# Kernel optimization log

Hardware: AMD Instinct MI355X
Metric: run time of the kernel (lower is better)

Reference implementation:

```python
import jax, jax.numpy as jnp
import numpy as np

NUM_HEADS = 8
ATTN_DIM = 64

def setup_inputs() -> dict:
    key = jax.random.key(0)
    ks = jax.random.split(key, 16)
    C = ATTN_DIM
    inp = {
        "rgb_fea": jax.random.normal(ks[0], (2, C, 48, 48), jnp.float32),
        "depth_fea": jax.random.normal(ks[1], (2, 1, 24, 24), jnp.float32),
        # expend_conv: Conv2d(1 -> C, k=1), with bias (torch default)
        "w_exp": jax.random.normal(ks[2], (C, 1), jnp.float32) * 0.2,
        "b_exp": jax.random.normal(ks[3], (C,), jnp.float32) * 0.02,
        # q/k/v linears (no bias), weights stored torch-style [out, in]
        "w_rgb_q": jax.random.normal(ks[4], (C, C), jnp.float32) * (C ** -0.5),
        "w_rgb_k": jax.random.normal(ks[5], (C, C), jnp.float32) * (C ** -0.5),
        "w_rgb_v": jax.random.normal(ks[6], (C, C), jnp.float32) * (C ** -0.5),
        "w_dep_q": jax.random.normal(ks[7], (C, C), jnp.float32) * (C ** -0.5),
        "w_dep_k": jax.random.normal(ks[8], (C, C), jnp.float32) * (C ** -0.5),
        "w_dep_v": jax.random.normal(ks[9], (C, C), jnp.float32) * (C ** -0.5),
        # output projections (with bias)
        "w_rgb_proj": jax.random.normal(ks[10], (C, C), jnp.float32) * (C ** -0.5),
        "b_rgb_proj": jax.random.normal(ks[11], (C,), jnp.float32) * 0.02,
        "w_dep_proj": jax.random.normal(ks[12], (C, C), jnp.float32) * (C ** -0.5),
        "b_dep_proj": jax.random.normal(ks[13], (C,), jnp.float32) * 0.02,
        # compress_conv: Conv2d(2C -> C, k=1), with bias
        "w_comp": jax.random.normal(ks[14], (C, 2 * C), jnp.float32) * ((2 * C) ** -0.5),
        "b_comp": jax.random.normal(ks[15], (C,), jnp.float32) * 0.02,
    }
    return inp


def _heads(x, b, n, h):
    # [B, N, C] -> [B, H, N, C/H]
    c = x.shape[-1]
    return x.reshape(b, n, h, c // h).transpose(0, 2, 1, 3)


def reference(rgb_fea, depth_fea, w_exp, b_exp,
              w_rgb_q, w_rgb_k, w_rgb_v, w_dep_q, w_dep_k, w_dep_v,
              w_rgb_proj, b_rgb_proj, w_dep_proj, b_dep_proj,
              w_comp, b_comp):
    b, c, h, w = rgb_fea.shape
    H = NUM_HEADS
    scale = (c // H) ** -0.5

    # expend_conv (1x1) + ReLU + bilinear upsample (align_corners=False)
    d = jnp.einsum('bihw,oi->bohw', depth_fea, w_exp) + b_exp[None, :, None, None]
    d = jax.nn.relu(d)
    d = jax.image.resize(d, (b, c, h, w), method='bilinear')

    # (B,C,H,W) -> transpose(1,3) -> (B,W,H,C) -> (B, N=w*h, C)
    N = w * h
    rgb = rgb_fea.transpose(0, 3, 2, 1).reshape(b, N, c)
    dep = d.transpose(0, 3, 2, 1).reshape(b, N, c)

    rq = _heads(rgb @ w_rgb_q.T, b, N, H)
    rk = _heads(rgb @ w_rgb_k.T, b, N, H)
    rv = _heads(rgb @ w_rgb_v.T, b, N, H)
    dq = _heads(dep @ w_dep_q.T, b, N, H)
    dk = _heads(dep @ w_dep_k.T, b, N, H)
    dv = _heads(dep @ w_dep_v.T, b, N, H)

    # rgb queries attend to depth keys/values
    rgb_attn = jax.nn.softmax(jnp.einsum('bhnd,bhmd->bhnm', rq, dk) * scale, axis=-1)
    rgb_out = jnp.einsum('bhnm,bhmd->bhnd', rgb_attn, dv)
    rgb_out = rgb_out.transpose(0, 2, 1, 3).reshape(b, N, c) @ w_rgb_proj.T + b_rgb_proj

    # depth queries attend to rgb keys/values
    dep_attn = jax.nn.softmax(jnp.einsum('bhnd,bhmd->bhnm', dq, rk) * scale, axis=-1)
    dep_out = jnp.einsum('bhnm,bhmd->bhnd', dep_attn, rv)
    dep_out = dep_out.transpose(0, 2, 1, 3).reshape(b, N, c) @ w_dep_proj.T + b_dep_proj

    # (B,N,C) -> (B,C,N) -> (B,C,w,h)
    rgb_out = rgb_out.transpose(0, 2, 1).reshape(b, c, w, h)
    dep_out = dep_out.transpose(0, 2, 1).reshape(b, c, w, h)

    fuse = jnp.concatenate([rgb_out, dep_out], axis=1)
    fuse = jnp.einsum('bihw,oi->bohw', fuse, w_comp) + b_comp[None, :, None, None]
    return jax.nn.gelu(fuse, approximate=False)
```

## Files before the change

kernel.cpp:

```cpp
#include <hip/hip_runtime.h>
#include <math.h>

#define BATCH 2
#define C 64
#define HH 48
#define WW 48
#define NTOK 2304
#define HEADS 8
#define KVSTRIDE 12

typedef unsigned short bf16_t;
typedef __attribute__((ext_vector_type(8))) short bf16x8;
typedef __attribute__((ext_vector_type(4))) short bf16x4;
typedef __attribute__((ext_vector_type(4))) float f32x4;

__device__ __forceinline__ bf16_t f2bf(float f) {
    unsigned int u = __float_as_uint(f);
    u = (u + 0x7fffu + ((u >> 16) & 1u)) >> 16;
    return (bf16_t)u;
}
__device__ __forceinline__ unsigned pack2(float a, float b) {
    return (unsigned)f2bf(a) | ((unsigned)f2bf(b) << 16);
}
__device__ __forceinline__ float4 ld_bf4(const bf16_t* p) {
    uint2 v = *(const uint2*)p;
    float4 r;
    r.x = __uint_as_float(v.x << 16); r.y = __uint_as_float(v.x & 0xffff0000u);
    r.z = __uint_as_float(v.y << 16); r.w = __uint_as_float(v.y & 0xffff0000u);
    return r;
}

__device__ __forceinline__ void stage_x_row(
    float* xrow, const float* rgb, const float* dep,
    const float* w_exp, const float* b_exp,
    int b, int n, int strm, int c0, int cstep)
{
    int wi = n / HH, hi = n % HH;
    if (strm == 0) {
        const float* base = rgb + (size_t)b * C * NTOK + (size_t)hi * WW + wi;
        for (int c = c0; c < 64; c += cstep)
            xrow[c] = base[(size_t)c * NTOK];
    } else {
        float cy = 0.5f * hi - 0.25f, cx = 0.5f * wi - 0.25f;
        float fy0 = floorf(cy), fx0 = floorf(cx);
        float fy = cy - fy0, fx = cx - fx0;
        int y0 = max((int)fy0, 0), x0 = max((int)fx0, 0);
        int y1 = min((int)fy0 + 1, 23), x1 = min((int)fx0 + 1, 23);
        const float* dp = dep + b * 576;
        float d00 = dp[y0*24 + x0], d01 = dp[y0*24 + x1];
        float d10 = dp[y1*24 + x0], d11 = dp[y1*24 + x1];
        for (int c = c0; c < 64; c += cstep) {
            float w = w_exp[c], bb = b_exp[c];
            float r00 = fmaxf(w*d00 + bb, 0.f), r01 = fmaxf(w*d01 + bb, 0.f);
            float r10 = fmaxf(w*d10 + bb, 0.f), r11 = fmaxf(w*d11 + bb, 0.f);
            xrow[c] = (1.f-fy)*((1.f-fx)*r00 + fx*r01) + fy*((1.f-fx)*r10 + fx*r11);
        }
    }
}


__global__ __launch_bounds__(256) void qkvprep_kernel(
    const float* __restrict__ rgb, const float* __restrict__ dep,
    const float* __restrict__ w_exp, const float* __restrict__ b_exp,
    const float* __restrict__ w_rq, const float* __restrict__ w_rk,
    const float* __restrict__ w_rv,
    const float* __restrict__ w_dq, const float* __restrict__ w_dk,
    const float* __restrict__ w_dv,
    const float* __restrict__ w_rp, const float* __restrict__ w_dp,
    const float* __restrict__ w_comp,
    const float* __restrict__ b_rp, const float* __restrict__ b_dp,
    const float* __restrict__ b_comp,
    bf16_t* __restrict__ Qb, bf16_t* __restrict__ Kb, bf16_t* __restrict__ VT,
    float* __restrict__ W1, float* __restrict__ W2, float* __restrict__ beff)
{
    __shared__ float Xs[16][68];
    __shared__ float Ws[64][68];
    int bxid = blockIdx.x;
    int tid = threadIdx.x;
    int sr = tid >> 4, sc = (tid & 15) * 4;

    if (bxid < 144) {
        int tile = bxid;
        int z = blockIdx.y;
        int b = z >> 1, strm = z & 1;
        int sb = strm*2 + b;

        float4 wreg[3][4];
        #pragma unroll
        for (int m = 0; m < 3; ++m) {
            const float* W = strm ? (m == 0 ? w_dq : m == 1 ? w_dk : w_dv)
                                  : (m == 0 ? w_rq : m == 1 ? w_rk : w_rv);
            #pragma unroll
            for (int rr = 0; rr < 4; ++rr)
                wreg[m][rr] = *(const float4*)&W[(rr*16 + sr)*64 + sc];
        }
        {
            int r = tid & 15, c0 = tid >> 4;
            stage_x_row(&Xs[r][0], rgb, dep, w_exp, b_exp,
                        b, tile*16 + r, strm, c0, 16);
        }

        int ty = tid >> 4, tx = tid & 15;
        #pragma unroll
        for (int m = 0; m < 3; ++m) {
            __syncthreads();
            #pragma unroll
            for (int rr = 0; rr < 4; ++rr)
                *(float4*)&Ws[rr*16 + sr][sc] = wreg[m][rr];
            __syncthreads();

            float acc[4] = {};
            #pragma unroll
            for (int k = 0; k < 64; k += 4) {
                float4 xv = *(const float4*)&Xs[ty][k];
                #pragma unroll
                for (int j = 0; j < 4; ++j) {
                    float4 wv = *(const float4*)&Ws[tx + 16*j][k];
                    acc[j] += xv.x*wv.x + xv.y*wv.y + xv.z*wv.z + xv.w*wv.w;
                }
            }
            float scale = (m == 0) ? (0.35355339059327373f * 1.4426950408889634f) : 1.0f;
            int n = tile*16 + ty;
            #pragma unroll
            for (int j = 0; j < 4; ++j) {
                int o = tx + 16*j;
                int h = o >> 3, d = o & 7;
                bf16_t v = f2bf(acc[j] * scale);
                if (m == 0)      Qb[(((size_t)sb*8 + h)*NTOK + n)*8 + d] = v;
                else if (m == 1) Kb[(((size_t)sb*8 + h)*NTOK + n)*8 + d] = v;
                else             VT[(((size_t)sb*8 + h)*8 + d)*NTOK + n] = v;
            }
        }
    } else {
        int m = bxid - 144;
        int bx = blockIdx.y;
        const float* Wp = m ? w_dp : w_rp;
        float* Wo = m ? W2 : W1;
        #pragma unroll
        for (int rr = 0; rr < 4; ++rr) {
            int r = rr*16 + sr;
            *(float4*)&Ws[r][sc] = *(const float4*)&Wp[r*64 + sc];
        }
        __syncthreads();
        int r = tid >> 4;
        int o = bx*16 + r;
        int c4 = (tid & 15) * 4;
        float a0 = 0, a1 = 0, a2 = 0, a3 = 0;
        for (int j = 0; j < 64; ++j) {
            float wc = w_comp[o*128 + m*64 + j];
            float4 wp = *(const float4*)&Ws[j][c4];
            a0 += wc*wp.x; a1 += wc*wp.y; a2 += wc*wp.z; a3 += wc*wp.w;
        }
        Wo[o*64 + c4]     = a0;
        Wo[o*64 + c4 + 1] = a1;
        Wo[o*64 + c4 + 2] = a2;
        Wo[o*64 + c4 + 3] = a3;
        if (m == 0 && bx == 0 && tid < 64) {
            float s = b_comp[tid];
            for (int j = 0; j < 64; ++j)
                s += w_comp[tid*128 + j] * b_rp[j] + w_comp[tid*128 + 64 + j] * b_dp[j];
            beff[tid] = s;
        }
    }
}

__global__ __launch_bounds__(256) void attn_kernel(
    const bf16_t* __restrict__ Qb, const bf16_t* __restrict__ Kb,
    const bf16_t* __restrict__ VT,
    float* __restrict__ AOr, float* __restrict__ AOd)
{
    int h = blockIdx.y;
    int z = blockIdx.z;
    int b = z >> 1, which = z & 1;
    int qsb = which * 2 + b;
    int ksb = (1 - which) * 2 + b;
    const bf16_t* Q  = Qb + ((size_t)qsb * 8 + h) * NTOK * 8;
    const bf16_t* K  = Kb + ((size_t)ksb * 8 + h) * NTOK * 8;
    const bf16_t* Vt = VT + ((size_t)ksb * 8 + h) * 8 * NTOK;
    float* AO = which ? AOd : AOr;

    __shared__ __align__(16) bf16_t Pls[4][16][40];
    __shared__ __align__(16) float  Ols[4][16][16];

    int tid = threadIdx.x;
    int t = tid & 63, w = tid >> 6;
    int m16 = t & 15, quad = t >> 4;
    int qt = blockIdx.x * 4 + w;
    int n0 = qt * 16;

    const bf16x8 zf = {0,0,0,0,0,0,0,0};
    const bf16x8 onesf = {0x3F80,0x3F80,0x3F80,0x3F80,
                          0x3F80,0x3F80,0x3F80,0x3F80};
    const f32x4 cz = {0.f, 0.f, 0.f, 0.f};

    bf16x8 qf = (quad == 0) ? *(const bf16x8*)&Q[(size_t)(n0 + m16) * 8] : zf;

    f32x4 oacc = cz;

    #pragma unroll 1
    for (int ck = 0; ck < 72; ++ck) {
        int k0 = ck * 32;
        bf16x8 kf0 = (quad == 0) ? *(const bf16x8*)&K[(size_t)(k0 + m16) * 8]      : zf;
        bf16x8 kf1 = (quad == 0) ? *(const bf16x8*)&K[(size_t)(k0 + 16 + m16) * 8] : zf;
        bf16x8 vf = (m16 < 8) ? *(const bf16x8*)&Vt[(size_t)m16 * NTOK + k0 + quad * 8]
                  : (m16 == 8 ? onesf : zf);

        f32x4 s0 = __builtin_amdgcn_mfma_f32_16x16x32_bf16(kf0, qf, cz, 0, 0, 0);
        f32x4 s1 = __builtin_amdgcn_mfma_f32_16x16x32_bf16(kf1, qf, cz, 0, 0, 0);

        bf16x4 pA, pB;
        #pragma unroll
        for (int r = 0; r < 4; ++r) {
            float p0 = __builtin_amdgcn_exp2f(s0[r]);
            float p1 = __builtin_amdgcn_exp2f(s1[r]);
            pA[r] = (short)(__float_as_uint(p0) >> 16);
            pB[r] = (short)(__float_as_uint(p1) >> 16);
        }
        *(bf16x4*)&Pls[w][m16][quad * 4]      = pA;
        *(bf16x4*)&Pls[w][m16][16 + quad * 4] = pB;

        bf16x8 pf = *(const bf16x8*)&Pls[w][m16][quad * 8];
        oacc = __builtin_amdgcn_mfma_f32_16x16x32_bf16(pf, vf, oacc, 0, 0, 0);
    }

    #pragma unroll
    for (int r = 0; r < 4; ++r)
        Ols[w][quad*4 + r][m16] = oacc[r];
    #pragma unroll
    for (int e = 0; e < 2; ++e) {
        int idx = t * 2 + e;
        int qq = idx >> 3, d = idx & 7;
        float val = Ols[w][qq][d] / Ols[w][qq][8];
        AO[((size_t)b * NTOK + n0 + qq) * 64 + 8 * h + d] = val;
    }
}

__global__ __launch_bounds__(256) void outcomp_kernel(
    const float* __restrict__ AOr, const float* __restrict__ AOd,
    const float* __restrict__ W1, const float* __restrict__ W2,
    const float* __restrict__ beff, float* __restrict__ out)
{
    int tile = blockIdx.x;
    int b    = blockIdx.y;
    int n0 = tile * 16;
    __shared__ float Ar[16][68];
    __shared__ float Ad[16][68];
    __shared__ float W1s[64][68];
    __shared__ float W2s[64][68];
    int tid = threadIdx.x;
    {
        int row = tid >> 4, c4 = (tid & 15) * 4;
        size_t base = (size_t)b*NTOK + n0 + row;
        *(float4*)&Ar[row][c4] = *(const float4*)&AOr[base*64 + c4];
        *(float4*)&Ad[row][c4] = *(const float4*)&AOd[base*64 + c4];
    }
    {
        int sr = tid >> 4, sc4 = (tid & 15) * 4;
        #pragma unroll
        for (int rr = 0; rr < 4; ++rr) {
            int r = rr*16 + sr;
            *(float4*)&W1s[r][sc4] = *(const float4*)&W1[r*64 + sc4];
            *(float4*)&W2s[r][sc4] = *(const float4*)&W2[r*64 + sc4];
        }
    }
    __syncthreads();

    int tx = tid & 15, ty = tid >> 4;
    float g[4] = {};
    #pragma unroll
    for (int k = 0; k < 64; k += 4) {
        float4 xr = *(const float4*)&Ar[ty][k];
        float4 xd = *(const float4*)&Ad[ty][k];
        #pragma unroll
        for (int jj = 0; jj < 4; ++jj) {
            float4 w1 = *(const float4*)&W1s[tx + 16*jj][k];
            float4 w2 = *(const float4*)&W2s[tx + 16*jj][k];
            g[jj] += xr.x*w1.x + xr.y*w1.y + xr.z*w1.z + xr.w*w1.w
                   + xd.x*w2.x + xd.y*w2.y + xd.z*w2.z + xd.w*w2.w;
        }
    }

    __syncthreads();
    float* Gs = &W1s[0][0];
    #pragma unroll
    for (int jj = 0; jj < 4; ++jj) {
        int o = tx + 16*jj;
        float x = g[jj] + beff[o];
        float gl = 0.5f * x * (1.0f + erff(x * 0.70710678118654752f));
        Gs[o*20 + ty] = gl;
    }
    __syncthreads();
    {
        int o = tid >> 2, s = tid & 3;
        float4 v = *(const float4*)&Gs[o*20 + 4*s];
        *(float4*)&out[((size_t)(b*C + o))*NTOK + n0 + 4*s] = v;
    }
}

__global__ __launch_bounds__(256) void kv_all_kernel(
    const float* __restrict__ rgb, const float* __restrict__ dep,
    const float* __restrict__ w_exp, const float* __restrict__ b_exp,
    const float* __restrict__ w_rk, const float* __restrict__ w_rv,
    const float* __restrict__ w_dk, const float* __restrict__ w_dv,
    bf16_t* __restrict__ Kr, bf16_t* __restrict__ Vr,
    bf16_t* __restrict__ Kd, bf16_t* __restrict__ Vd)
{
    int tile = blockIdx.x;
    int m    = blockIdx.y;
    int z    = blockIdx.z;
    int b = z >> 1, strm = z & 1;
    const float* W = strm ? (m ? w_dv : w_dk) : (m ? w_rv : w_rk);
    bf16_t* O = (strm ? (m ? Vd : Kd) : (m ? Vr : Kr))
              + ((size_t)b * NTOK + tile * 64) * 64;

    __shared__ float Xs[64][68];
    __shared__ float Ws[64][68];
    int tid = threadIdx.x;
    {
        int r = tid & 63, c0 = tid >> 6;
        stage_x_row(&Xs[r][0], rgb, dep, w_exp, b_exp, b, tile*64 + r, strm, c0, 4);
    }
    int sr = tid >> 4, sc = (tid & 15) * 4;
    #pragma unroll
    for (int rr = 0; rr < 4; ++rr) {
        int r = rr*16 + sr;
        *(float4*)&Ws[r][sc] = *(const float4*)&W[r*64 + sc];
    }
    __syncthreads();

    int ty = tid >> 4, tx = tid & 15;
    float acc[4][4] = {};
    #pragma unroll
    for (int k = 0; k < 64; k += 4) {
        float4 xv[4], wv4[4];
        #pragma unroll
        for (int i = 0; i < 4; ++i) xv[i] = *(const float4*)&Xs[4*ty + i][k];
        #pragma unroll
        for (int j = 0; j < 4; ++j) wv4[j] = *(const float4*)&Ws[tx + 16*j][k];
        #pragma unroll
        for (int i = 0; i < 4; ++i)
            #pragma unroll
            for (int j = 0; j < 4; ++j)
                acc[i][j] += xv[i].x*wv4[j].x + xv[i].y*wv4[j].y + xv[i].z*wv4[j].z + xv[i].w*wv4[j].w;
    }
    #pragma unroll
    for (int i = 0; i < 4; ++i)
        #pragma unroll
        for (int j = 0; j < 4; ++j)
            O[(4*ty + i)*64 + tx + 16*j] = f2bf(acc[i][j]);
}

__global__ __launch_bounds__(256) void attn_all_kernel(
    const float* __restrict__ rgb, const float* __restrict__ dep,
    const float* __restrict__ w_exp, const float* __restrict__ b_exp,
    const float* __restrict__ w_rq, const float* __restrict__ w_dq,
    const bf16_t* __restrict__ Kr, const bf16_t* __restrict__ Vr,
    const bf16_t* __restrict__ Kd, const bf16_t* __restrict__ Vd,
    bf16_t* __restrict__ AOr, bf16_t* __restrict__ AOd)
{
    int qt = blockIdx.x;
    int h  = blockIdx.y;
    int z  = blockIdx.z;
    int b = z >> 1, which = z & 1;
    const float* wq = which ? w_dq : w_rq;
    const bf16_t* K = which ? Kr : Kd;
    const bf16_t* V = which ? Vr : Vd;
    bf16_t* AO      = which ? AOd : AOr;

    __shared__ float Xs[64][68];
    __shared__ float Wqs[8][64];
    __shared__ __align__(16) float Ks[4][64][KVSTRIDE];
    __shared__ __align__(16) float Vs[4][64][KVSTRIDE];

    int tid = threadIdx.x;
    int t = tid & 63;
    int w = tid >> 6;
    int n = qt * 64 + t;

    stage_x_row(&Xs[t][0], rgb, dep, w_exp, b_exp, b, n, which == 0 ? 0 : 1, w, 4);
    if (w == 0) {
        #pragma unroll
        for (int d = 0; d < 8; ++d) Wqs[d][t] = wq[(8*h + d)*64 + t];
    }
    __syncthreads();

    const float sc = 0.35355339059327373f * 1.4426950408889634f;
    float q[8];
    #pragma unroll
    for (int d = 0; d < 8; ++d) {
        float s = 0.f;
        #pragma unroll 8
        for (int c = 0; c < 64; ++c) s += Xs[t][c] * Wqs[d][c];
        q[d] = s * sc;
    }

    float mrun = -INFINITY, l = 0.f;
    float acc[8] = {};

    #pragma unroll 1
    for (int st = 0; st < 9; ++st) {
        __syncthreads();
        {
            size_t g = ((size_t)b * NTOK + (w*576 + st*64 + t)) * 64 + 8 * h;
            *(float4*)&Ks[w][t][0] = ld_bf4(&K[g]);
            *(float4*)&Ks[w][t][4] = ld_bf4(&K[g + 4]);
            *(float4*)&Vs[w][t][0] = ld_bf4(&V[g]);
            *(float4*)&Vs[w][t][4] = ld_bf4(&V[g + 4]);
        }
        __syncthreads();

        for (int g8 = 0; g8 < 8; ++g8) {
            float s[8];
            #pragma unroll
            for (int u = 0; u < 8; ++u) {
                const float4 ka = *(const float4*)&Ks[w][g8*8 + u][0];
                const float4 kb = *(const float4*)&Ks[w][g8*8 + u][4];
                s[u] = q[0]*ka.x + q[1]*ka.y + q[2]*ka.z + q[3]*ka.w
                     + q[4]*kb.x + q[5]*kb.y + q[6]*kb.z + q[7]*kb.w;
            }
            float tm = fmaxf(fmaxf(fmaxf(s[0],s[1]), fmaxf(s[2],s[3])),
                             fmaxf(fmaxf(s[4],s[5]), fmaxf(s[6],s[7])));
            float mn = fmaxf(mrun, tm);
            float alpha = __builtin_amdgcn_exp2f(mrun - mn);
            float ps = 0.f;
            #pragma unroll
            for (int u = 0; u < 8; ++u) { s[u] = __builtin_amdgcn_exp2f(s[u] - mn); ps += s[u]; }
            l = l * alpha + ps;
            #pragma unroll
            for (int d = 0; d < 8; ++d) acc[d] *= alpha;
            #pragma unroll
            for (int u = 0; u < 8; ++u) {
                const float4 va = *(const float4*)&Vs[w][g8*8 + u][0];
                const float4 vb = *(const float4*)&Vs[w][g8*8 + u][4];
                acc[0] += s[u]*va.x; acc[1] += s[u]*va.y; acc[2] += s[u]*va.z; acc[3] += s[u]*va.w;
                acc[4] += s[u]*vb.x; acc[5] += s[u]*vb.y; acc[6] += s[u]*vb.z; acc[7] += s[u]*vb.w;
            }
            mrun = mn;
        }
    }

    float* part = &Xs[0][0];
    __syncthreads();
    {
        float* p = &part[(w*64 + t) * 10];
        p[0] = mrun; p[1] = l;
        #pragma unroll
        for (int d = 0; d < 8; ++d) p[2 + d] = acc[d];
    }
    __syncthreads();
    if (tid < 64) {
        float M = -INFINITY;
        #pragma unroll
        for (int v = 0; v < 4; ++v) M = fmaxf(M, part[(v*64 + t)*10]);
        float L = 0.f, o[8] = {};
        #pragma unroll
        for (int v = 0; v < 4; ++v) {
            const float* p = &part[(v*64 + t)*10];
            float al = __builtin_amdgcn_exp2f(p[0] - M);
            L += p[1] * al;
            #pragma unroll
            for (int d = 0; d < 8; ++d) o[d] += p[2 + d] * al;
        }
        float inv = 1.0f / L;
        uint4 ov;
        ov.x = pack2(o[0]*inv, o[1]*inv);
        ov.y = pack2(o[2]*inv, o[3]*inv);
        ov.z = pack2(o[4]*inv, o[5]*inv);
        ov.w = pack2(o[6]*inv, o[7]*inv);
        *(uint4*)&AO[((size_t)b * NTOK + n) * 64 + 8 * h] = ov;
    }
}

__global__ __launch_bounds__(256) void projcomp_all_kernel(
    const bf16_t* __restrict__ AOr, const bf16_t* __restrict__ AOd,
    const float* __restrict__ w_rp, const float* __restrict__ b_rp,
    const float* __restrict__ w_dp, const float* __restrict__ b_dp,
    const float* __restrict__ w_comp, const float* __restrict__ b_comp,
    float* __restrict__ out)
{
    int tile = blockIdx.x;
    int b    = blockIdx.y;
    __shared__ float A[64][68];
    __shared__ float Bf[64][68];
    __shared__ float Pf[64][68];
    int tid = threadIdx.x;
    int sr = tid >> 4, sc = (tid & 15) * 4;
    int ty = tid >> 4, tx = tid & 15;
    float G[4][4] = {};

    #pragma unroll
    for (int half = 0; half < 2; ++half) {
        const bf16_t* AOx = half ? AOd : AOr;
        const float* Wp   = half ? w_dp : w_rp;
        const float* bp   = half ? b_dp : b_rp;
        #pragma unroll
        for (int rr = 0; rr < 4; ++rr) {
            int r = rr*16 + sr;
            *(float4*)&A[r][sc]  = ld_bf4(&AOx[((size_t)b*NTOK + tile*64 + r)*64 + sc]);
            *(float4*)&Bf[r][sc] = *(const float4*)&Wp[r*64 + sc];
        }
        __syncthreads();
        float acc[4][4] = {};
        #pragma unroll
        for (int k = 0; k < 64; k += 4) {
            float4 xv[4], wv[4];
            #pragma unroll
            for (int i = 0; i < 4; ++i) xv[i] = *(const float4*)&A[4*ty + i][k];
            #pragma unroll
            for (int j = 0; j < 4; ++j) wv[j] = *(const float4*)&Bf[tx + 16*j][k];
            #pragma unroll
            for (int i = 0; i < 4; ++i)
                #pragma unroll
                for (int j = 0; j < 4; ++j)
                    acc[i][j] += xv[i].x*wv[j].x + xv[i].y*wv[j].y + xv[i].z*wv[j].z + xv[i].w*wv[j].w;
        }
        __syncthreads();
        #pragma unroll
        for (int j = 0; j < 4; ++j) {
            float bj = bp[tx + 16*j];
            #pragma unroll
            for (int i = 0; i < 4; ++i)
                Pf[4*ty + i][tx + 16*j] = acc[i][j] + bj;
        }
        #pragma unroll
        for (int rr = 0; rr < 4; ++rr) {
            int r = rr*16 + sr;
            *(float4*)&Bf[r][sc] = *(const float4*)&w_comp[r*128 + half*64 + sc];
        }
        __syncthreads();
        #pragma unroll
        for (int k = 0; k < 64; k += 4) {
            float4 xv[4], wv[4];
            #pragma unroll
            for (int i = 0; i < 4; ++i) xv[i] = *(const float4*)&Pf[4*ty + i][k];
            #pragma unroll
            for (int j = 0; j < 4; ++j) wv[j] = *(const float4*)&Bf[tx + 16*j][k];
            #pragma unroll
            for (int i = 0; i < 4; ++i)
                #pragma unroll
                for (int j = 0; j < 4; ++j)
                    G[i][j] += xv[i].x*wv[j].x + xv[i].y*wv[j].y + xv[i].z*wv[j].z + xv[i].w*wv[j].w;
        }
        __syncthreads();
    }

    #pragma unroll
    for (int j = 0; j < 4; ++j) {
        int o = tx + 16*j;
        float bj = b_comp[o];
        #pragma unroll
        for (int i = 0; i < 4; ++i) {
            int n = tile*64 + 4*ty + i;
            int wi = n / HH, hi = n % HH;
            float x = G[i][j] + bj;
            float g = 0.5f * x * (1.0f + erff(x * 0.70710678118654752f));
            out[((b*C + o)*WW + wi)*HH + hi] = g;
        }
    }
}

extern "C" void kernel_launch(void* const* d_in, const int* in_sizes, int n_in,
                              void* d_out, int out_size, void* d_ws, size_t ws_size,
                              hipStream_t stream) {
    const float* rgb_fea = (const float*)d_in[0];
    const float* depth   = (const float*)d_in[1];
    const float* w_exp   = (const float*)d_in[2];
    const float* b_exp   = (const float*)d_in[3];
    const float* w_rq    = (const float*)d_in[4];
    const float* w_rk    = (const float*)d_in[5];
    const float* w_rv    = (const float*)d_in[6];
    const float* w_dq    = (const float*)d_in[7];
    const float* w_dk    = (const float*)d_in[8];
    const float* w_dv    = (const float*)d_in[9];
    const float* w_rp    = (const float*)d_in[10];
    const float* b_rp    = (const float*)d_in[11];
    const float* w_dp    = (const float*)d_in[12];
    const float* b_dp    = (const float*)d_in[13];
    const float* w_comp  = (const float*)d_in[14];
    const float* b_comp  = (const float*)d_in[15];
    float* out = (float*)d_out;

    if (ws_size >= 5931264) {
        char* Wb = (char*)d_ws;
        bf16_t* Qb   = (bf16_t*)Wb;
        bf16_t* Kb   = (bf16_t*)(Wb + 1179648);
        bf16_t* VT   = (bf16_t*)(Wb + 2359296);
        float*  AOr  = (float*)(Wb + 3538944);
        float*  AOd  = AOr + 294912;
        float*  W1   = (float*)(Wb + 5898240);
        float*  W2   = (float*)(Wb + 5914624);
        float*  beff = (float*)(Wb + 5931008);

        qkvprep_kernel<<<dim3(146, 4), dim3(256), 0, stream>>>(
            rgb_fea, depth, w_exp, b_exp,
            w_rq, w_rk, w_rv, w_dq, w_dk, w_dv,
            w_rp, w_dp, w_comp, b_rp, b_dp, b_comp,
            Qb, Kb, VT, W1, W2, beff);
        attn_kernel<<<dim3(36, 8, 4), dim3(256), 0, stream>>>(
            Qb, Kb, VT, AOr, AOd);
        outcomp_kernel<<<dim3(144, 2), dim3(256), 0, stream>>>(
            AOr, AOd, W1, W2, beff, out);
    } else {
        const size_t BUF = (size_t)BATCH * NTOK * 64;
        bf16_t* Kr  = (bf16_t*)d_ws;
        bf16_t* Vr  = Kr + BUF;
        bf16_t* Kd  = Vr + BUF;
        bf16_t* Vd  = Kd + BUF;
        bf16_t* AOr = Vd + BUF;
        bf16_t* AOd = AOr + BUF;
        kv_all_kernel<<<dim3(36, 2, 4), dim3(256), 0, stream>>>(
            rgb_fea, depth, w_exp, b_exp, w_rk, w_rv, w_dk, w_dv, Kr, Vr, Kd, Vd);
        attn_all_kernel<<<dim3(36, 8, 4), dim3(256), 0, stream>>>(
            rgb_fea, depth, w_exp, b_exp, w_rq, w_dq, Kr, Vr, Kd, Vd, AOr, AOd);
        projcomp_all_kernel<<<dim3(36, 2), dim3(256), 0, stream>>>(
            AOr, AOd, w_rp, b_rp, w_dp, b_dp, w_comp, b_comp, out);
    }
}
```

Measured before the change: 161.3 us.

## Split QKV prep across grid z and unroll attention loop by two chunks

The QKV prep kernel now spreads the three projections (Q, K, V) over blockIdx.z, so each block computes a single projection with one weight-staging pass. Launch is 145x4x3, and the former two extra weight-fold blocks are remapped to block 144 with z<2. The attention kernel processes 64 keys per iteration, with double P buffers in LDS, to give more independent MFMA and exp work per loop trip. This adds more blocks that each restage the X rows, and raises register and LDS use in attention.

```diff
diff --git a/kernel.cpp b/kernel.cpp
--- a/kernel.cpp
+++ b/kernel.cpp
@@ -82,57 +82,48 @@
     if (bxid < 144) {
         int tile = bxid;
         int z = blockIdx.y;
+        int m = blockIdx.z;
         int b = z >> 1, strm = z & 1;
         int sb = strm*2 + b;
-
-        float4 wreg[3][4];
-        #pragma unroll
-        for (int m = 0; m < 3; ++m) {
-            const float* W = strm ? (m == 0 ? w_dq : m == 1 ? w_dk : w_dv)
-                                  : (m == 0 ? w_rq : m == 1 ? w_rk : w_rv);
-            #pragma unroll
-            for (int rr = 0; rr < 4; ++rr)
-                wreg[m][rr] = *(const float4*)&W[(rr*16 + sr)*64 + sc];
+        const float* W = strm ? (m == 0 ? w_dq : m == 1 ? w_dk : w_dv)
+                              : (m == 0 ? w_rq : m == 1 ? w_rk : w_rv);
+
+        #pragma unroll
+        for (int rr = 0; rr < 4; ++rr) {
+            int r = rr*16 + sr;
+            *(float4*)&Ws[r][sc] = *(const float4*)&W[r*64 + sc];
         }
         {
             int r = tid & 15, c0 = tid >> 4;
             stage_x_row(&Xs[r][0], rgb, dep, w_exp, b_exp,
                         b, tile*16 + r, strm, c0, 16);
         }
+        __syncthreads();
 
         int ty = tid >> 4, tx = tid & 15;
-        #pragma unroll
-        for (int m = 0; m < 3; ++m) {
-            __syncthreads();
-            #pragma unroll
-            for (int rr = 0; rr < 4; ++rr)
-                *(float4*)&Ws[rr*16 + sr][sc] = wreg[m][rr];
-            __syncthreads();
-
-            float acc[4] = {};
-            #pragma unroll
-            for (int k = 0; k < 64; k += 4) {
-                float4 xv = *(const float4*)&Xs[ty][k];
-                #pragma unroll
-                for (int j = 0; j < 4; ++j) {
-                    float4 wv = *(const float4*)&Ws[tx + 16*j][k];
-                    acc[j] += xv.x*wv.x + xv.y*wv.y + xv.z*wv.z + xv.w*wv.w;
-                }
+        float acc[4] = {};
+        #pragma unroll
+        for (int k = 0; k < 64; k += 4) {
+            float4 xv = *(const float4*)&Xs[ty][k];
+            #pragma unroll
+            for (int j = 0; j < 4; ++j) {
+                float4 wv = *(const float4*)&Ws[tx + 16*j][k];
+                acc[j] += xv.x*wv.x + xv.y*wv.y + xv.z*wv.z + xv.w*wv.w;
             }
-            float scale = (m == 0) ? (0.35355339059327373f * 1.4426950408889634f) : 1.0f;
-            int n = tile*16 + ty;
-            #pragma unroll
-            for (int j = 0; j < 4; ++j) {
-                int o = tx + 16*j;
-                int h = o >> 3, d = o & 7;
-                bf16_t v = f2bf(acc[j] * scale);
-                if (m == 0)      Qb[(((size_t)sb*8 + h)*NTOK + n)*8 + d] = v;
-                else if (m == 1) Kb[(((size_t)sb*8 + h)*NTOK + n)*8 + d] = v;
-                else             VT[(((size_t)sb*8 + h)*8 + d)*NTOK + n] = v;
-            }
-        }
-    } else {
-        int m = bxid - 144;
+        }
+        float scale = (m == 0) ? (0.35355339059327373f * 1.4426950408889634f) : 1.0f;
+        int n = tile*16 + ty;
+        #pragma unroll
+        for (int j = 0; j < 4; ++j) {
+            int o = tx + 16*j;
+            int h = o >> 3, d = o & 7;
+            bf16_t v = f2bf(acc[j] * scale);
+            if (m == 0)      Qb[(((size_t)sb*8 + h)*NTOK + n)*8 + d] = v;
+            else if (m == 1) Kb[(((size_t)sb*8 + h)*NTOK + n)*8 + d] = v;
+            else             VT[(((size_t)sb*8 + h)*8 + d)*NTOK + n] = v;
+        }
+    } else if (blockIdx.z < 2) {
+        int m = blockIdx.z;
         int bx = blockIdx.y;
         const float* Wp = m ? w_dp : w_rp;
         float* Wo = m ? W2 : W1;
@@ -179,7 +170,7 @@
     const bf16_t* Vt = VT + ((size_t)ksb * 8 + h) * 8 * NTOK;
     float* AO = which ? AOd : AOr;
 
-    __shared__ __align__(16) bf16_t Pls[4][16][40];
+    __shared__ __align__(16) bf16_t Pls[4][2][16][40];
     __shared__ __align__(16) float  Ols[4][16][16];
 
     int tid = threadIdx.x;
@@ -192,35 +183,51 @@
     const bf16x8 onesf = {0x3F80,0x3F80,0x3F80,0x3F80,
                           0x3F80,0x3F80,0x3F80,0x3F80};
     const f32x4 cz = {0.f, 0.f, 0.f, 0.f};
+    bf16_t* PA = &Pls[w][0][0][0];
+    bf16_t* PB = &Pls[w][1][0][0];
 
     bf16x8 qf = (quad == 0) ? *(const bf16x8*)&Q[(size_t)(n0 + m16) * 8] : zf;
 
     f32x4 oacc = cz;
 
     #pragma unroll 1
-    for (int ck = 0; ck < 72; ++ck) {
-        int k0 = ck * 32;
-        bf16x8 kf0 = (quad == 0) ? *(const bf16x8*)&K[(size_t)(k0 + m16) * 8]      : zf;
-        bf16x8 kf1 = (quad == 0) ? *(const bf16x8*)&K[(size_t)(k0 + 16 + m16) * 8] : zf;
-        bf16x8 vf = (m16 < 8) ? *(const bf16x8*)&Vt[(size_t)m16 * NTOK + k0 + quad * 8]
+    for (int ck = 0; ck < 36; ++ck) {
+        int k0 = ck * 64;
+        bf16x8 kA0 = (quad == 0) ? *(const bf16x8*)&K[(size_t)(k0 + m16) * 8]      : zf;
+        bf16x8 kA1 = (quad == 0) ? *(const bf16x8*)&K[(size_t)(k0 + 16 + m16) * 8] : zf;
+        bf16x8 kB0 = (quad == 0) ? *(const bf16x8*)&K[(size_t)(k0 + 32 + m16) * 8] : zf;
+        bf16x8 kB1 = (quad == 0) ? *(const bf16x8*)&K[(size_t)(k0 + 48 + m16) * 8] : zf;
+        bf16x8 vA = (m16 < 8) ? *(const bf16x8*)&Vt[(size_t)m16 * NTOK + k0 + quad * 8]
                   : (m16 == 8 ? onesf : zf);
-
-        f32x4 s0 = __builtin_amdgcn_mfma_f32_16x16x32_bf16(kf0, qf, cz, 0, 0, 0);
-        f32x4 s1 = __builtin_amdgcn_mfma_f32_16x16x32_bf16(kf1, qf, cz, 0, 0, 0);
-
-        bf16x4 pA, pB;
+        bf16x8 vB = (m16 < 8) ? *(const bf16x8*)&Vt[(size_t)m16 * NTOK + k0 + 32 + quad * 8]
+                  : (m16 == 8 ? onesf : zf);
+
+        f32x4 sA0 = __builtin_amdgcn_mfma_f32_16x16x32_bf16(kA0, qf, cz, 0, 0, 0);
+        f32x4 sA1 = __builtin_amdgcn_mfma_f32_16x16x32_bf16(kA1, qf, cz, 0, 0, 0);
+        f32x4 sB0 = __builtin_amdgcn_mfma_f32_16x16x32_bf16(kB0, qf, cz, 0, 0, 0);
+        f32x4 sB1 = __builtin_amdgcn_mfma_f32_16x16x32_bf16(kB1, qf, cz, 0, 0, 0);
+
+        bf16x4 pA0, pA1, pB0, pB1;
         #pragma unroll
         for (int r = 0; r < 4; ++r) {
-            float p0 = __builtin_amdgcn_exp2f(s0[r]);
-            float p1 = __builtin_amdgcn_exp2f(s1[r]);
-            pA[r] = (short)(__float_as_uint(p0) >> 16);
-            pB[r] = (short)(__float_as_uint(p1) >> 16);
-        }
-        *(bf16x4*)&Pls[w][m16][quad * 4]      = pA;
-        *(bf16x4*)&Pls[w][m16][16 + quad * 4] = pB;
-
-        bf16x8 pf = *(const bf16x8*)&Pls[w][m16][quad * 8];
-        oacc = __builtin_amdgcn_mfma_f32_16x16x32_bf16(pf, vf, oacc, 0, 0, 0);
+            float a0 = __builtin_amdgcn_exp2f(sA0[r]);
+            float a1 = __builtin_amdgcn_exp2f(sA1[r]);
+            float b0 = __builtin_amdgcn_exp2f(sB0[r]);
+            float b1 = __builtin_amdgcn_exp2f(sB1[r]);
+            pA0[r] = (short)(__float_as_uint(a0) >> 16);
+            pA1[r] = (short)(__float_as_uint(a1) >> 16);
+            pB0[r] = (short)(__float_as_uint(b0) >> 16);
+            pB1[r] = (short)(__float_as_uint(b1) >> 16);
+        }
+        *(bf16x4*)&PA[m16*40 + quad * 4]      = pA0;
+        *(bf16x4*)&PA[m16*40 + 16 + quad * 4] = pA1;
+        *(bf16x4*)&PB[m16*40 + quad * 4]      = pB0;
+        *(bf16x4*)&PB[m16*40 + 16 + quad * 4] = pB1;
+
+        bf16x8 pfA = *(const bf16x8*)&PA[m16*40 + quad * 8];
+        oacc = __builtin_amdgcn_mfma_f32_16x16x32_bf16(pfA, vA, oacc, 0, 0, 0);
+        bf16x8 pfB = *(const bf16x8*)&PB[m16*40 + quad * 8];
+        oacc = __builtin_amdgcn_mfma_f32_16x16x32_bf16(pfB, vB, oacc, 0, 0, 0);
     }
 
     #pragma unroll
@@ -591,7 +598,7 @@
         float*  W2   = (float*)(Wb + 5914624);
         float*  beff = (float*)(Wb + 5931008);
 
-        qkvprep_kernel<<<dim3(146, 4), dim3(256), 0, stream>>>(
+        qkvprep_kernel<<<dim3(145, 4, 3), dim3(256), 0, stream>>>(
             rgb_fea, depth, w_exp, b_exp,
             w_rq, w_rk, w_rv, w_dq, w_dk, w_dv,
             w_rp, w_dp, w_comp, b_rp, b_dp, b_comp,
```

Result: slower. 167.0 us (+3.5%).

## Fuse output projection and GELU into attention via last-arriver counters

Applied to the files above, without the earlier changes.

Removes the separate outcomp kernel. Each attention wave increments a per-(batch, query-tile) atomic counter, and the 16th arriver (8 heads × 2 directions) performs the folded projection, compress conv and GELU for that 16-token tile. Counters are zeroed in the prep kernel, which now also splits the Q/K/V projections across a third grid dimension so each block computes one matrix. This saves a kernel launch and its tail, at the cost of atomics, fences, and a scalar per-wave epilogue that reads weights from global memory.

```diff
diff --git a/kernel.cpp b/kernel.cpp
--- a/kernel.cpp
+++ b/kernel.cpp
@@ -71,7 +71,8 @@
     const float* __restrict__ b_rp, const float* __restrict__ b_dp,
     const float* __restrict__ b_comp,
     bf16_t* __restrict__ Qb, bf16_t* __restrict__ Kb, bf16_t* __restrict__ VT,
-    float* __restrict__ W1, float* __restrict__ W2, float* __restrict__ beff)
+    float* __restrict__ W1, float* __restrict__ W2, float* __restrict__ beff,
+    unsigned* __restrict__ cnt)
 {
     __shared__ float Xs[16][68];
     __shared__ float Ws[64][68];
@@ -82,57 +83,48 @@
     if (bxid < 144) {
         int tile = bxid;
         int z = blockIdx.y;
+        int m = blockIdx.z;
         int b = z >> 1, strm = z & 1;
         int sb = strm*2 + b;
-
-        float4 wreg[3][4];
-        #pragma unroll
-        for (int m = 0; m < 3; ++m) {
-            const float* W = strm ? (m == 0 ? w_dq : m == 1 ? w_dk : w_dv)
-                                  : (m == 0 ? w_rq : m == 1 ? w_rk : w_rv);
-            #pragma unroll
-            for (int rr = 0; rr < 4; ++rr)
-                wreg[m][rr] = *(const float4*)&W[(rr*16 + sr)*64 + sc];
+        const float* W = strm ? (m == 0 ? w_dq : m == 1 ? w_dk : w_dv)
+                              : (m == 0 ? w_rq : m == 1 ? w_rk : w_rv);
+
+        #pragma unroll
+        for (int rr = 0; rr < 4; ++rr) {
+            int r = rr*16 + sr;
+            *(float4*)&Ws[r][sc] = *(const float4*)&W[r*64 + sc];
         }
         {
             int r = tid & 15, c0 = tid >> 4;
             stage_x_row(&Xs[r][0], rgb, dep, w_exp, b_exp,
                         b, tile*16 + r, strm, c0, 16);
         }
+        __syncthreads();
 
         int ty = tid >> 4, tx = tid & 15;
-        #pragma unroll
-        for (int m = 0; m < 3; ++m) {
-            __syncthreads();
-            #pragma unroll
-            for (int rr = 0; rr < 4; ++rr)
-                *(float4*)&Ws[rr*16 + sr][sc] = wreg[m][rr];
-            __syncthreads();
-
-            float acc[4] = {};
-            #pragma unroll
-            for (int k = 0; k < 64; k += 4) {
-                float4 xv = *(const float4*)&Xs[ty][k];
-                #pragma unroll
-                for (int j = 0; j < 4; ++j) {
-                    float4 wv = *(const float4*)&Ws[tx + 16*j][k];
-                    acc[j] += xv.x*wv.x + xv.y*wv.y + xv.z*wv.z + xv.w*wv.w;
-                }
+        float acc[4] = {};
+        #pragma unroll
+        for (int k = 0; k < 64; k += 4) {
+            float4 xv = *(const float4*)&Xs[ty][k];
+            #pragma unroll
+            for (int j = 0; j < 4; ++j) {
+                float4 wv = *(const float4*)&Ws[tx + 16*j][k];
+                acc[j] += xv.x*wv.x + xv.y*wv.y + xv.z*wv.z + xv.w*wv.w;
             }
-            float scale = (m == 0) ? (0.35355339059327373f * 1.4426950408889634f) : 1.0f;
-            int n = tile*16 + ty;
-            #pragma unroll
-            for (int j = 0; j < 4; ++j) {
-                int o = tx + 16*j;
-                int h = o >> 3, d = o & 7;
-                bf16_t v = f2bf(acc[j] * scale);
-                if (m == 0)      Qb[(((size_t)sb*8 + h)*NTOK + n)*8 + d] = v;
-                else if (m == 1) Kb[(((size_t)sb*8 + h)*NTOK + n)*8 + d] = v;
-                else             VT[(((size_t)sb*8 + h)*8 + d)*NTOK + n] = v;
-            }
-        }
-    } else {
-        int m = bxid - 144;
+        }
+        float scale = (m == 0) ? (0.35355339059327373f * 1.4426950408889634f) : 1.0f;
+        int n = tile*16 + ty;
+        #pragma unroll
+        for (int j = 0; j < 4; ++j) {
+            int o = tx + 16*j;
+            int h = o >> 3, d = o & 7;
+            bf16_t v = f2bf(acc[j] * scale);
+            if (m == 0)      Qb[(((size_t)sb*8 + h)*NTOK + n)*8 + d] = v;
+            else if (m == 1) Kb[(((size_t)sb*8 + h)*NTOK + n)*8 + d] = v;
+            else             VT[(((size_t)sb*8 + h)*8 + d)*NTOK + n] = v;
+        }
+    } else if (blockIdx.z < 2) {
+        int m = blockIdx.z;
         int bx = blockIdx.y;
         const float* Wp = m ? w_dp : w_rp;
         float* Wo = m ? W2 : W1;
@@ -161,13 +153,19 @@
                 s += w_comp[tid*128 + j] * b_rp[j] + w_comp[tid*128 + 64 + j] * b_dp[j];
             beff[tid] = s;
         }
-    }
-}
-
-__global__ __launch_bounds__(256) void attn_kernel(
+    } else if (blockIdx.y == 0) {
+        for (int i = tid; i < 288; i += 256) cnt[i] = 0;
+    }
+}
+
+__global__ __launch_bounds__(256) void attnout_kernel(
     const bf16_t* __restrict__ Qb, const bf16_t* __restrict__ Kb,
     const bf16_t* __restrict__ VT,
-    float* __restrict__ AOr, float* __restrict__ AOd)
+    float* __restrict__ AOr, float* __restrict__ AOd,
+    const float* __restrict__ W1, const float* __restrict__ W2,
+    const float* __restrict__ beff,
+    unsigned* __restrict__ cnt,
+    float* __restrict__ out)
 {
     int h = blockIdx.y;
     int z = blockIdx.z;
@@ -233,67 +231,46 @@
         float val = Ols[w][qq][d] / Ols[w][qq][8];
         AO[((size_t)b * NTOK + n0 + qq) * 64 + 8 * h + d] = val;
     }
-}
-
-__global__ __launch_bounds__(256) void outcomp_kernel(
-    const float* __restrict__ AOr, const float* __restrict__ AOd,
-    const float* __restrict__ W1, const float* __restrict__ W2,
-    const float* __restrict__ beff, float* __restrict__ out)
-{
-    int tile = blockIdx.x;
-    int b    = blockIdx.y;
-    int n0 = tile * 16;
-    __shared__ float Ar[16][68];
-    __shared__ float Ad[16][68];
-    __shared__ float W1s[64][68];
-    __shared__ float W2s[64][68];
-    int tid = threadIdx.x;
-    {
-        int row = tid >> 4, c4 = (tid & 15) * 4;
-        size_t base = (size_t)b*NTOK + n0 + row;
-        *(float4*)&Ar[row][c4] = *(const float4*)&AOr[base*64 + c4];
-        *(float4*)&Ad[row][c4] = *(const float4*)&AOd[base*64 + c4];
-    }
-    {
-        int sr = tid >> 4, sc4 = (tid & 15) * 4;
-        #pragma unroll
-        for (int rr = 0; rr < 4; ++rr) {
-            int r = rr*16 + sr;
-            *(float4*)&W1s[r][sc4] = *(const float4*)&W1[r*64 + sc4];
-            *(float4*)&W2s[r][sc4] = *(const float4*)&W2[r*64 + sc4];
-        }
-    }
-    __syncthreads();
-
-    int tx = tid & 15, ty = tid >> 4;
-    float g[4] = {};
-    #pragma unroll
-    for (int k = 0; k < 64; k += 4) {
-        float4 xr = *(const float4*)&Ar[ty][k];
-        float4 xd = *(const float4*)&Ad[ty][k];
-        #pragma unroll
-        for (int jj = 0; jj < 4; ++jj) {
-            float4 w1 = *(const float4*)&W1s[tx + 16*jj][k];
-            float4 w2 = *(const float4*)&W2s[tx + 16*jj][k];
-            g[jj] += xr.x*w1.x + xr.y*w1.y + xr.z*w1.z + xr.w*w1.w
-                   + xd.x*w2.x + xd.y*w2.y + xd.z*w2.z + xd.w*w2.w;
-        }
-    }
-
-    __syncthreads();
-    float* Gs = &W1s[0][0];
-    #pragma unroll
-    for (int jj = 0; jj < 4; ++jj) {
-        int o = tx + 16*jj;
-        float x = g[jj] + beff[o];
-        float gl = 0.5f * x * (1.0f + erff(x * 0.70710678118654752f));
-        Gs[o*20 + ty] = gl;
-    }
-    __syncthreads();
-    {
-        int o = tid >> 2, s = tid & 3;
-        float4 v = *(const float4*)&Gs[o*20 + 4*s];
-        *(float4*)&out[((size_t)(b*C + o))*NTOK + n0 + 4*s] = v;
+
+    __threadfence();
+    int last = 0;
+    if (t == 0) {
+        unsigned old = __hip_atomic_fetch_add(&cnt[b * 144 + qt], 1u,
+                           __ATOMIC_ACQ_REL, __HIP_MEMORY_SCOPE_AGENT);
+        last = (old == 15u);
+    }
+    last = __shfl(last, 0);
+    if (!last) return;
+    __threadfence();
+
+    int tok = t & 15, kg = t >> 4;
+    const float* ar = &AOr[((size_t)b * NTOK + n0 + tok) * 64 + kg * 16];
+    const float* ad = &AOd[((size_t)b * NTOK + n0 + tok) * 64 + kg * 16];
+    float xr[16], xd[16];
+    #pragma unroll
+    for (int i = 0; i < 16; i += 4) {
+        *(float4*)&xr[i] = *(const float4*)&ar[i];
+        *(float4*)&xd[i] = *(const float4*)&ad[i];
+    }
+    #pragma unroll 1
+    for (int o = 0; o < 64; ++o) {
+        const float* w1 = &W1[o * 64 + kg * 16];
+        const float* w2 = &W2[o * 64 + kg * 16];
+        float p = 0.f;
+        #pragma unroll
+        for (int i = 0; i < 16; i += 4) {
+            float4 wv1 = *(const float4*)&w1[i];
+            float4 wv2 = *(const float4*)&w2[i];
+            p += xr[i]*wv1.x + xr[i+1]*wv1.y + xr[i+2]*wv1.z + xr[i+3]*wv1.w
+               + xd[i]*wv2.x + xd[i+1]*wv2.y + xd[i+2]*wv2.z + xd[i+3]*wv2.w;
+        }
+        p += __shfl_xor(p, 16);
+        p += __shfl_xor(p, 32);
+        if (kg == (o & 3)) {
+            float x = p + beff[o];
+            float gl = 0.5f * x * (1.0f + erff(x * 0.70710678118654752f));
+            out[((size_t)(b * C + o)) * NTOK + n0 + tok] = gl;
+        }
     }
 }
 
@@ -580,7 +557,7 @@
     const float* b_comp  = (const float*)d_in[15];
     float* out = (float*)d_out;
 
-    if (ws_size >= 5931264) {
+    if (ws_size >= 5932416) {
         char* Wb = (char*)d_ws;
         bf16_t* Qb   = (bf16_t*)Wb;
         bf16_t* Kb   = (bf16_t*)(Wb + 1179648);
@@ -590,16 +567,15 @@
         float*  W1   = (float*)(Wb + 5898240);
         float*  W2   = (float*)(Wb + 5914624);
         float*  beff = (float*)(Wb + 5931008);
-
-        qkvprep_kernel<<<dim3(146, 4), dim3(256), 0, stream>>>(
+        unsigned* cnt = (unsigned*)(Wb + 5931264);
+
+        qkvprep_kernel<<<dim3(145, 4, 3), dim3(256), 0, stream>>>(
             rgb_fea, depth, w_exp, b_exp,
             w_rq, w_rk, w_rv, w_dq, w_dk, w_dv,
             w_rp, w_dp, w_comp, b_rp, b_dp, b_comp,
-            Qb, Kb, VT, W1, W2, beff);
-        attn_kernel<<<dim3(36, 8, 4), dim3(256), 0, stream>>>(
-            Qb, Kb, VT, AOr, AOd);
-        outcomp_kernel<<<dim3(144, 2), dim3(256), 0, stream>>>(
-            AOr, AOd, W1, W2, beff, out);
+            Qb, Kb, VT, W1, W2, beff, cnt);
+        attnout_kernel<<<dim3(36, 8, 4), dim3(256), 0, stream>>>(
+            Qb, Kb, VT, AOr, AOd, W1, W2, beff, cnt, out);
     } else {
         const size_t BUF = (size_t)BATCH * NTOK * 64;
         bf16_t* Kr  = (bf16_t*)d_ws;
```

Result: slower. 394.5 us (+144.5%).

## Split attention key range across two blocks and merge partials in output kernel

Applied to the files above, without the earlier changes.

Adds a split-K variant of the attention kernel in which each query tile's key loop is divided between two blocks. Each block writes an unnormalized partial output and its row sum, and a new output kernel adds the two partials and normalizes before the projection and GELU. The aim is to double the grid and shorten the serial 72-iteration key loop so the GPU is better occupied. In exchange it writes and reads extra global partial buffers and needs a larger workspace. It is only used when that workspace is available.

```diff
diff --git a/kernel.cpp b/kernel.cpp
--- a/kernel.cpp
+++ b/kernel.cpp
@@ -164,10 +164,11 @@
     }
 }
 
-__global__ __launch_bounds__(256) void attn_kernel(
+template<bool SPLIT>
+__global__ __launch_bounds__(256) void attn_kernel_t(
     const bf16_t* __restrict__ Qb, const bf16_t* __restrict__ Kb,
     const bf16_t* __restrict__ VT,
-    float* __restrict__ AOr, float* __restrict__ AOd)
+    float* __restrict__ AOall, float* __restrict__ Lall)
 {
     int h = blockIdx.y;
     int z = blockIdx.z;
@@ -177,7 +178,6 @@
     const bf16_t* Q  = Qb + ((size_t)qsb * 8 + h) * NTOK * 8;
     const bf16_t* K  = Kb + ((size_t)ksb * 8 + h) * NTOK * 8;
     const bf16_t* Vt = VT + ((size_t)ksb * 8 + h) * 8 * NTOK;
-    float* AO = which ? AOd : AOr;
 
     __shared__ __align__(16) bf16_t Pls[4][16][40];
     __shared__ __align__(16) float  Ols[4][16][16];
@@ -185,7 +185,11 @@
     int tid = threadIdx.x;
     int t = tid & 63, w = tid >> 6;
     int m16 = t & 15, quad = t >> 4;
-    int qt = blockIdx.x * 4 + w;
+
+    int qt, kh, ck0;
+    if (SPLIT) { qt = (blockIdx.x >> 1) * 4 + w; kh = blockIdx.x & 1; ck0 = kh * 36; }
+    else       { qt = blockIdx.x * 4 + w;        kh = 0;              ck0 = 0; }
+    int nck = SPLIT ? 36 : 72;
     int n0 = qt * 16;
 
     const bf16x8 zf = {0,0,0,0,0,0,0,0};
@@ -198,8 +202,8 @@
     f32x4 oacc = cz;
 
     #pragma unroll 1
-    for (int ck = 0; ck < 72; ++ck) {
-        int k0 = ck * 32;
+    for (int ci = 0; ci < nck; ++ci) {
+        int k0 = (ck0 + ci) * 32;
         bf16x8 kf0 = (quad == 0) ? *(const bf16x8*)&K[(size_t)(k0 + m16) * 8]      : zf;
         bf16x8 kf1 = (quad == 0) ? *(const bf16x8*)&K[(size_t)(k0 + 16 + m16) * 8] : zf;
         bf16x8 vf = (m16 < 8) ? *(const bf16x8*)&Vt[(size_t)m16 * NTOK + k0 + quad * 8]
@@ -226,12 +230,27 @@
     #pragma unroll
     for (int r = 0; r < 4; ++r)
         Ols[w][quad*4 + r][m16] = oacc[r];
-    #pragma unroll
-    for (int e = 0; e < 2; ++e) {
-        int idx = t * 2 + e;
-        int qq = idx >> 3, d = idx & 7;
-        float val = Ols[w][qq][d] / Ols[w][qq][8];
-        AO[((size_t)b * NTOK + n0 + qq) * 64 + 8 * h + d] = val;
+
+    if (SPLIT) {
+        float* AO = AOall + (size_t)(kh*2 + which) * BATCH * NTOK * 64;
+        float* Lx = Lall  + (size_t)(kh*2 + which) * BATCH * NTOK * 8;
+        #pragma unroll
+        for (int e = 0; e < 2; ++e) {
+            int idx = t * 2 + e;
+            int qq = idx >> 3, d = idx & 7;
+            AO[((size_t)b * NTOK + n0 + qq) * 64 + 8 * h + d] = Ols[w][qq][d];
+        }
+        if (t < 16)
+            Lx[((size_t)b * NTOK + n0 + t) * 8 + h] = Ols[w][t][8];
+    } else {
+        float* AO = AOall + (size_t)which * BATCH * NTOK * 64;
+        #pragma unroll
+        for (int e = 0; e < 2; ++e) {
+            int idx = t * 2 + e;
+            int qq = idx >> 3, d = idx & 7;
+            float val = Ols[w][qq][d] / Ols[w][qq][8];
+            AO[((size_t)b * NTOK + n0 + qq) * 64 + 8 * h + d] = val;
+        }
     }
 }
 
@@ -253,6 +272,83 @@
         size_t base = (size_t)b*NTOK + n0 + row;
         *(float4*)&Ar[row][c4] = *(const float4*)&AOr[base*64 + c4];
         *(float4*)&Ad[row][c4] = *(const float4*)&AOd[base*64 + c4];
+    }
+    {
+        int sr = tid >> 4, sc4 = (tid & 15) * 4;
+        #pragma unroll
+        for (int rr = 0; rr < 4; ++rr) {
+            int r = rr*16 + sr;
+            *(float4*)&W1s[r][sc4] = *(const float4*)&W1[r*64 + sc4];
+            *(float4*)&W2s[r][sc4] = *(const float4*)&W2[r*64 + sc4];
+        }
+    }
+    __syncthreads();
+
+    int tx = tid & 15, ty = tid >> 4;
+    float g[4] = {};
+    #pragma unroll
+    for (int k = 0; k < 64; k += 4) {
+        float4 xr = *(const float4*)&Ar[ty][k];
+        float4 xd = *(const float4*)&Ad[ty][k];
+        #pragma unroll
+        for (int jj = 0; jj < 4; ++jj) {
+            float4 w1 = *(const float4*)&W1s[tx + 16*jj][k];
+            float4 w2 = *(const float4*)&W2s[tx + 16*jj][k];
+            g[jj] += xr.x*w1.x + xr.y*w1.y + xr.z*w1.z + xr.w*w1.w
+                   + xd.x*w2.x + xd.y*w2.y + xd.z*w2.z + xd.w*w2.w;
+        }
+    }
+
+    __syncthreads();
+    float* Gs = &W1s[0][0];
+    #pragma unroll
+    for (int jj = 0; jj < 4; ++jj) {
+        int o = tx + 16*jj;
+        float x = g[jj] + beff[o];
+        float gl = 0.5f * x * (1.0f + erff(x * 0.70710678118654752f));
+        Gs[o*20 + ty] = gl;
+    }
+    __syncthreads();
+    {
+        int o = tid >> 2, s = tid & 3;
+        float4 v = *(const float4*)&Gs[o*20 + 4*s];
+        *(float4*)&out[((size_t)(b*C + o))*NTOK + n0 + 4*s] = v;
+    }
+}
+
+__global__ __launch_bounds__(256) void outcomp2_kernel(
+    const float* __restrict__ AOall, const float* __restrict__ Lall,
+    const float* __restrict__ W1, const float* __restrict__ W2,
+    const float* __restrict__ beff, float* __restrict__ out)
+{
+    int tile = blockIdx.x;
+    int b    = blockIdx.y;
+    int n0 = tile * 16;
+    __shared__ float Ar[16][68];
+    __shared__ float Ad[16][68];
+    __shared__ float W1s[64][68];
+    __shared__ float W2s[64][68];
+    int tid = threadIdx.x;
+    {
+        const size_t S  = (size_t)BATCH * NTOK * 64;
+        const size_t SL = (size_t)BATCH * NTOK * 8;
+        int row = tid >> 4, c4 = (tid & 15) * 4;
+        size_t base = (size_t)b*NTOK + n0 + row;
+        int hh = c4 >> 3;
+        float4 r0 = *(const float4*)&AOall[0*S + base*64 + c4];
+        float4 r1 = *(const float4*)&AOall[2*S + base*64 + c4];
+        float4 d0 = *(const float4*)&AOall[1*S + base*64 + c4];
+        float4 d1 = *(const float4*)&AOall[3*S + base*64 + c4];
+        float lr = Lall[0*SL + base*8 + hh] + Lall[2*SL + base*8 + hh];
+        float ld = Lall[1*SL + base*8 + hh] + Lall[3*SL + base*8 + hh];
+        float ir = 1.0f / lr, id = 1.0f / ld;
+        float4 vr, vd;
+        vr.x = (r0.x + r1.x) * ir; vr.y = (r0.y + r1.y) * ir;
+        vr.z = (r0.z + r1.z) * ir; vr.w = (r0.w + r1.w) * ir;
+        vd.x = (d0.x + d1.x) * id; vd.y = (d0.y + d1.y) * id;
+        vd.z = (d0.z + d1.z) * id; vd.w = (d0.w + d1.w) * id;
+        *(float4*)&Ar[row][c4] = vr;
+        *(float4*)&Ad[row][c4] = vd;
     }
     {
         int sr = tid >> 4, sc4 = (tid & 15) * 4;
@@ -580,7 +676,27 @@
     const float* b_comp  = (const float*)d_in[15];
     float* out = (float*)d_out;
 
-    if (ws_size >= 5931264) {
+    if (ws_size >= 8880384) {
+        char* Wb = (char*)d_ws;
+        bf16_t* Qb    = (bf16_t*)Wb;
+        bf16_t* Kb    = (bf16_t*)(Wb + 1179648);
+        bf16_t* VT    = (bf16_t*)(Wb + 2359296);
+        float*  AOall = (float*)(Wb + 3538944);
+        float*  Lall  = (float*)(Wb + 8257536);
+        float*  W1    = (float*)(Wb + 8847360);
+        float*  W2    = (float*)(Wb + 8863744);
+        float*  beff  = (float*)(Wb + 8880128);
+
+        qkvprep_kernel<<<dim3(146, 4), dim3(256), 0, stream>>>(
+            rgb_fea, depth, w_exp, b_exp,
+            w_rq, w_rk, w_rv, w_dq, w_dk, w_dv,
+            w_rp, w_dp, w_comp, b_rp, b_dp, b_comp,
+            Qb, Kb, VT, W1, W2, beff);
+        attn_kernel_t<true><<<dim3(72, 8, 4), dim3(256), 0, stream>>>(
+            Qb, Kb, VT, AOall, Lall);
+        outcomp2_kernel<<<dim3(144, 2), dim3(256), 0, stream>>>(
+            AOall, Lall, W1, W2, beff, out);
+    } else if (ws_size >= 5931264) {
         char* Wb = (char*)d_ws;
         bf16_t* Qb   = (bf16_t*)Wb;
         bf16_t* Kb   = (bf16_t*)(Wb + 1179648);
@@ -596,8 +712,8 @@
             w_rq, w_rk, w_rv, w_dq, w_dk, w_dv,
             w_rp, w_dp, w_comp, b_rp, b_dp, b_comp,
             Qb, Kb, VT, W1, W2, beff);
-        attn_kernel<<<dim3(36, 8, 4), dim3(256), 0, stream>>>(
-            Qb, Kb, VT, AOr, AOd);
+        attn_kernel_t<false><<<dim3(36, 8, 4), dim3(256), 0, stream>>>(
+            Qb, Kb, VT, AOr, (float*)nullptr);
         outcomp_kernel<<<dim3(144, 2), dim3(256), 0, stream>>>(
             AOr, AOd, W1, W2, beff, out);
     } else {
```

After: 165.5 us. 1.03x slower.
